# Optimization experiments

Measured on AMD Instinct MI355X. Metric: run time of the kernel, lower is better.

Reference implementation:

```python
import jax, jax.numpy as jnp
import numpy as np

B, T, C, H = 4, 2048, 1024, 16
HD = C // H


def setup_inputs() -> dict:
    key = jax.random.key(0)
    k1, k2, k3 = jax.random.split(key, 3)
    x = jax.random.normal(k1, (B, T, C), dtype=jnp.float32)
    w_attn = jax.random.normal(k2, (C, 3 * C), dtype=jnp.float32) * (1.0 / np.sqrt(C))
    b_attn = jnp.zeros((3 * C,), dtype=jnp.float32)
    w_proj = jax.random.normal(k3, (C, C), dtype=jnp.float32) * (1.0 / np.sqrt(C))
    b_proj = jnp.zeros((C,), dtype=jnp.float32)
    return {"x": x, "w_attn": w_attn, "b_attn": b_attn, "w_proj": w_proj, "b_proj": b_proj}


def reference(x, w_attn, b_attn, w_proj, b_proj):
    # QKV projection: [B,T,3C]
    qkv = x @ w_attn + b_attn
    q, k, v = jnp.split(qkv, 3, axis=-1)
    # [B,H,T,HD]
    q = q.reshape(B, T, H, HD).swapaxes(1, 2)
    k = k.reshape(B, T, H, HD).swapaxes(1, 2)
    v = v.reshape(B, T, H, HD).swapaxes(1, 2)
    scale = 1.0 / jnp.sqrt(jnp.float32(HD))
    attn = jnp.einsum('bhqd,bhkd->bhqk', q, k) * scale  # [B,H,T,T]
    causal = jnp.tril(jnp.ones((T, T), dtype=bool))
    attn = jnp.where(causal[None, None, :, :], attn, -jnp.inf)
    attn = jax.nn.softmax(attn, axis=-1)
    y = jnp.einsum('bhqk,bhkd->bhqd', attn, v)  # [B,H,T,HD]
    y = y.swapaxes(1, 2).reshape(B, T, C)
    return y @ w_proj + b_proj
```

## Files before the change

kernel.cpp:

```cpp
#include <hip/hip_runtime.h>
#include <hip/hip_bf16.h>

#define BB 4
#define TT 2048
#define CC 1024
#define HH 16
#define HD 64
#define NQ (3*CC)
#define QSCALE 0.18033688011112042f

typedef __attribute__((ext_vector_type(8))) short bf16x8;
typedef __attribute__((ext_vector_type(4))) short short4_t;
typedef __attribute__((ext_vector_type(4))) float f32x4;

#define MFMA(a,b,c) __builtin_amdgcn_mfma_f32_16x16x32_bf16(a,b,c,0,0,0)

#define ASYNC16(gsrc, ldst) \
  __builtin_amdgcn_global_load_lds((const __attribute__((address_space(1))) void*)(gsrc), \
                                   (__attribute__((address_space(3))) void*)(ldst), 16, 0, 0)

#define SWZA(row) (((((row) & 7) + (((row) >> 3) & 3)) & 7) << 3)

static __device__ __forceinline__ short f2bf(float f){
    union { float f; unsigned u; } v; v.f = f;
    unsigned r = v.u + 0x7FFFu + ((v.u >> 16) & 1u);
    return (short)(r >> 16);
}
static __device__ __forceinline__ unsigned cvtpk(float a, float b){
    unsigned r;
    asm("v_cvt_pk_bf16_f32 %0, %1, %2" : "=v"(r) : "v"(a), "v"(b));
    return r;
}

__global__ __launch_bounds__(256)
void convert_x(const float* __restrict__ x, short* __restrict__ xb)
{
    int i = (blockIdx.x * 256 + threadIdx.x) * 8;
    float4 a = *reinterpret_cast<const float4*>(&x[i]);
    float4 b = *reinterpret_cast<const float4*>(&x[i+4]);
    bf16x8 o = { f2bf(a.x), f2bf(a.y), f2bf(a.z), f2bf(a.w),
                 f2bf(b.x), f2bf(b.y), f2bf(b.z), f2bf(b.w) };
    *reinterpret_cast<bf16x8*>(&xb[i]) = o;
}

__global__ __launch_bounds__(256)
void transpose_w(const float* __restrict__ w, short* __restrict__ wT, int N)
{
    __shared__ short sm[64*72];
    const int kt0 = blockIdx.x * 64;
    const int nt0 = blockIdx.y * 64;
    const int t = threadIdx.x;
    const int r  = t >> 4;
    const int c4 = (t & 15) * 4;
#pragma unroll
    for (int it = 0; it < 4; it++){
        int k = r + it*16;
        float4 v = *reinterpret_cast<const float4*>(&w[(size_t)(kt0 + k)*N + nt0 + c4]);
        sm[(c4+0)*72 + k] = f2bf(v.x);
        sm[(c4+1)*72 + k] = f2bf(v.y);
        sm[(c4+2)*72 + k] = f2bf(v.z);
        sm[(c4+3)*72 + k] = f2bf(v.w);
    }
    __syncthreads();
    const int nl = t >> 2;
    const int kc = (t & 3) * 16;
    bf16x8 o0 = *reinterpret_cast<const bf16x8*>(&sm[nl*72 + kc]);
    bf16x8 o1 = *reinterpret_cast<const bf16x8*>(&sm[nl*72 + kc + 8]);
    short* dst = &wT[(size_t)(nt0 + nl)*CC + kt0 + kc];
    *reinterpret_cast<bf16x8*>(dst)     = o0;
    *reinterpret_cast<bf16x8*>(dst + 8) = o1;
}

__global__ __launch_bounds__(256)
void transpose_v(const short* __restrict__ vb, short* __restrict__ vtb)
{
    __shared__ short sm[64*72];
    const int bh = blockIdx.x;
    const int t0 = blockIdx.y * 64;
    const int t = threadIdx.x;
    const int r   = t >> 2;
    const int c16 = (t & 3) * 16;
    const short* src = vb + (size_t)bh*TT*HD + (size_t)t0*HD;
    bf16x8 a0 = *reinterpret_cast<const bf16x8*>(&src[r*HD + c16]);
    bf16x8 a1 = *reinterpret_cast<const bf16x8*>(&src[r*HD + c16 + 8]);
#pragma unroll
    for (int j=0;j<8;j++){
        sm[(c16+j)*72 + r]   = a0[j];
        sm[(c16+8+j)*72 + r] = a1[j];
    }
    __syncthreads();
    bf16x8 o0 = *reinterpret_cast<const bf16x8*>(&sm[r*72 + c16]);
    bf16x8 o1 = *reinterpret_cast<const bf16x8*>(&sm[r*72 + c16 + 8]);
    short* dst = vtb + (size_t)bh*HD*TT + (size_t)r*TT + t0 + c16;
    *reinterpret_cast<bf16x8*>(dst)     = o0;
    *reinterpret_cast<bf16x8*>(dst + 8) = o1;
}

__global__ __launch_bounds__(256, 2)
void qkv_gemm(const short* __restrict__ xb, const short* __restrict__ wT,
              const float* __restrict__ bias,
              short* __restrict__ qb, short* __restrict__ kb, short* __restrict__ vb)
{
    __shared__ short As[128*64];
    __shared__ short Bs[128*64];
    const int bid = blockIdx.x;
    const int swz = (bid & 7) * 192 + (bid >> 3);
    const int bm = swz / (NQ/128);
    const int bn = swz % (NQ/128);
    const int m0 = bm*128, n0 = bn*128;
    const int t  = threadIdx.x;
    const int wid = t >> 6, lane = t & 63;
    const int wr = wid >> 1, wc = wid & 1;
    const int l15 = lane & 15, lh = lane >> 4;

    f32x4 acc[4][4];
#pragma unroll
    for (int i=0;i<4;i++)
#pragma unroll
      for (int j=0;j<4;j++) acc[i][j] = (f32x4)0.f;

    for (int k0 = 0; k0 < CC; k0 += 64) {
        __syncthreads();
#pragma unroll
        for (int i=0;i<4;i++){
            int u   = (wid*4 + i)*64 + lane;
            int row = u >> 3, c = u & 7;
            int cs  = c ^ (row & 7);
            ASYNC16(&xb[(size_t)(m0+row)*CC + k0 + cs*8], &As[(wid*4+i)*512]);
            ASYNC16(&wT[(size_t)(n0+row)*CC + k0 + cs*8], &Bs[(wid*4+i)*512]);
        }
        __syncthreads();
#pragma unroll
        for (int ks=0;ks<2;ks++){
            bf16x8 a[4], b[4];
#pragma unroll
            for (int m=0;m<4;m++){
                int row = wr*64 + m*16 + l15;
                a[m] = *reinterpret_cast<const bf16x8*>(&As[row*64 + (((ks<<2)|lh) ^ (row&7))*8]);
            }
#pragma unroll
            for (int n=0;n<4;n++){
                int col = wc*64 + n*16 + l15;
                b[n] = *reinterpret_cast<const bf16x8*>(&Bs[col*64 + (((ks<<2)|lh) ^ (col&7))*8]);
            }
#pragma unroll
            for (int m=0;m<4;m++)
#pragma unroll
              for (int n=0;n<4;n++)
                acc[m][n] = MFMA(a[m], b[n], acc[m][n]);
        }
    }

#pragma unroll
    for (int n=0;n<4;n++){
        int col = n0 + wc*64 + n*16 + l15;
        int sect = col >> 10;
        int cc = col & 1023;
        int h = cc >> 6, d = cc & 63;
        float bv = bias[col];
        short* dst = (sect==0) ? qb : (sect==1) ? kb : vb;
        float mul = (sect==0) ? QSCALE : 1.f;
#pragma unroll
        for (int m=0;m<4;m++)
#pragma unroll
          for (int r=0;r<4;r++){
            int row = m0 + wr*64 + m*16 + lh*4 + r;
            int b_ = row >> 11, tt_ = row & (TT-1);
            float v = (acc[m][n][r] + bv) * mul;
            dst[((size_t)(b_*HH + h)*TT + tt_)*HD + d] = f2bf(v);
          }
    }
}

__global__ __launch_bounds__(256, 3)
void attn_kernel(const short* __restrict__ qb, const short* __restrict__ kb,
                 const short* __restrict__ vtb, short* __restrict__ yb)
{
    __shared__ short Ks[2][64*64];
    __shared__ short Vt[2][64*64];
    __shared__ short Ps[4][32*64];

    const int bh = blockIdx.x;
    const int qt = 15 - blockIdx.y;
    const int b_ = bh >> 4, h = bh & 15;
    const short* qp  = qb  + (size_t)bh*TT*HD;
    const short* kp  = kb  + (size_t)bh*TT*HD;
    const short* vtp = vtb + (size_t)bh*HD*TT;
    const int t = threadIdx.x, wid = t >> 6, lane = t & 63;
    const int l15 = lane & 15, lh = lane >> 4;

    int kvoffB[8];
#pragma unroll
    for (int ks=0;ks<2;ks++)
#pragma unroll
      for (int i=0;i<4;i++){
        int row = i*16 + l15;
        kvoffB[ks*4+i] = ((row*64 + ks*32 + lh*8) ^ SWZA(row)) * 2;
      }
    int pwB[8];
#pragma unroll
    for (int m=0;m<2;m++){
        int qloc = m*16 + l15;
#pragma unroll
        for (int f=0;f<4;f++)
            pwB[m*4+f] = ((qloc*64 + f*16 + lh*4) ^ SWZA(qloc)) * 2;
    }
    char* KsB = (char*)&Ks[0][0];
    char* VtB = (char*)&Vt[0][0];
    char* PsB = (char*)&Ps[wid][0];

    const int su0 = (wid*2+0)*64 + lane;
    const int su1 = (wid*2+1)*64 + lane;
    const int sr0 = su0 >> 3, sc0 = (su0 & 7) ^ (SWZA(su0 >> 3) >> 3);
    const int sr1 = su1 >> 3, sc1 = (su1 & 7) ^ (SWZA(su1 >> 3) >> 3);

    const short* kg0 = kp  + (size_t)sr0*HD + sc0*8;
    const short* kg1 = kp  + (size_t)sr1*HD + sc1*8;
    const short* vg0 = vtp + (size_t)sr0*TT + sc0*8;
    const short* vg1 = vtp + (size_t)sr1*TT + sc1*8;

    const bf16x8 ones = { 0x3F80,0x3F80,0x3F80,0x3F80,0x3F80,0x3F80,0x3F80,0x3F80 };

    auto stageN = [&](int buf){
        ASYNC16(kg0, &Ks[buf][(wid*2+0)*512]);
        ASYNC16(kg1, &Ks[buf][(wid*2+1)*512]);
        ASYNC16(vg0, &Vt[buf][(wid*2+0)*512]);
        ASYNC16(vg1, &Vt[buf][(wid*2+1)*512]);
        kg0 += 64*HD; kg1 += 64*HD; vg0 += 64; vg1 += 64;
    };

    const int wq0 = qt*128 + wid*32;

    bf16x8 qf[2][2];
#pragma unroll
    for (int m=0;m<2;m++)
#pragma unroll
      for (int ks=0;ks<2;ks++)
        qf[m][ks] = *reinterpret_cast<const bf16x8*>(
            &qp[(size_t)(wq0 + m*16 + l15)*HD + ks*32 + lh*8]);

    f32x4 po[2][4];
    f32x4 pden[2];
#pragma unroll
    for (int m=0;m<2;m++){
        pden[m] = (f32x4)0.f;
#pragma unroll
        for (int n=0;n<4;n++) po[m][n] = (f32x4)0.f;
    }

    const int ntk = 2*(qt + 1);

    stageN(0);
    __syncthreads();

    for (int kt = 0; kt < ntk; ){
#pragma unroll
        for (int cur = 0; cur < 2; cur++, kt++){
            const int kv0 = kt*64;
            if (kt+1 < ntk) stageN(cur ^ 1);

            if (kv0 <= wq0 + 31){
                f32x4 s[2][4];
#pragma unroll
                for (int m=0;m<2;m++)
#pragma unroll
                  for (int f=0;f<4;f++) s[m][f] = (f32x4)0.f;
                __builtin_amdgcn_s_setprio(1);
#pragma unroll
                for (int ks=0;ks<2;ks++){
#pragma unroll
                    for (int f=0;f<4;f++){
                        bf16x8 kf = *reinterpret_cast<const bf16x8*>(
                            KsB + cur*8192 + kvoffB[ks*4+f]);
                        s[0][f] = MFMA(kf, qf[0][ks], s[0][f]);
                        s[1][f] = MFMA(kf, qf[1][ks], s[1][f]);
                    }
                }
                __builtin_amdgcn_s_setprio(0);
#pragma unroll
                for (int m=0;m<2;m++){
                    if (kv0 + 63 > wq0 + m*16){
                        int qm = wq0 + m*16 + l15;
#pragma unroll
                        for (int f=0;f<4;f++)
#pragma unroll
                          for (int r=0;r<4;r++){
                            int kv = kv0 + f*16 + lh*4 + r;
                            if (kv > qm) s[m][f][r] = -1e30f;
                          }
                    }
                }
#pragma unroll
                for (int m=0;m<2;m++){
#pragma unroll
                    for (int f=0;f<4;f++){
                        uint2 pk;
                        pk.x = cvtpk(exp2f(s[m][f][0]), exp2f(s[m][f][1]));
                        pk.y = cvtpk(exp2f(s[m][f][2]), exp2f(s[m][f][3]));
                        *reinterpret_cast<uint2*>(PsB + pwB[m*4+f]) = pk;
                    }
                }
                __builtin_amdgcn_s_setprio(1);
#pragma unroll
                for (int k2=0;k2<2;k2++){
                    bf16x8 pa[2];
#pragma unroll
                    for (int m=0;m<2;m++)
                        pa[m] = *reinterpret_cast<const bf16x8*>(PsB + kvoffB[k2*4+m]);
                    pden[0] = MFMA(pa[0], ones, pden[0]);
                    pden[1] = MFMA(pa[1], ones, pden[1]);
#pragma unroll
                    for (int n=0;n<4;n++){
                        bf16x8 vf = *reinterpret_cast<const bf16x8*>(
                            VtB + cur*8192 + kvoffB[k2*4+n]);
                        po[0][n] = MFMA(pa[0], vf, po[0][n]);
                        po[1][n] = MFMA(pa[1], vf, po[1][n]);
                    }
                }
                __builtin_amdgcn_s_setprio(0);
            }

            __syncthreads();
        }
    }

#pragma unroll
    for (int m=0;m<2;m++){
        float rcp[4];
#pragma unroll
        for (int r=0;r<4;r++) rcp[r] = 1.f / pden[m][r];
#pragma unroll
        for (int n=0;n<4;n++)
#pragma unroll
          for (int r=0;r<4;r++){
            int q = wq0 + m*16 + lh*4 + r;
            int dd = n*16 + l15;
            yb[(size_t)(b_*TT + q)*CC + h*HD + dd] = f2bf(po[m][n][r] * rcp[r]);
          }
    }
}

__global__ __launch_bounds__(256, 2)
void proj_gemm(const short* __restrict__ y, const short* __restrict__ wpT,
               const float* __restrict__ bias, float* __restrict__ out)
{
    __shared__ short As[128*64];
    __shared__ short Bs[128*64];
    const int bid = blockIdx.x;
    const int swz = (bid & 7) * 64 + (bid >> 3);
    const int bm = swz >> 3, bn = swz & 7;
    const int m0 = bm*128, n0 = bn*128;
    const int t  = threadIdx.x;
    const int wid = t >> 6, lane = t & 63;
    const int wr = wid >> 1, wc = wid & 1;
    const int l15 = lane & 15, lh = lane >> 4;

    f32x4 acc[4][4];
#pragma unroll
    for (int i=0;i<4;i++)
#pragma unroll
      for (int j=0;j<4;j++) acc[i][j] = (f32x4)0.f;

    for (int k0 = 0; k0 < CC; k0 += 64) {
        __syncthreads();
#pragma unroll
        for (int i=0;i<4;i++){
            int u   = (wid*4 + i)*64 + lane;
            int row = u >> 3, c = u & 7;
            int cs  = c ^ (row & 7);
            ASYNC16(&y[(size_t)(m0+row)*CC + k0 + cs*8],   &As[(wid*4+i)*512]);
            ASYNC16(&wpT[(size_t)(n0+row)*CC + k0 + cs*8], &Bs[(wid*4+i)*512]);
        }
        __syncthreads();
#pragma unroll
        for (int ks=0;ks<2;ks++){
            bf16x8 a[4], b[4];
#pragma unroll
            for (int m=0;m<4;m++){
                int row = wr*64 + m*16 + l15;
                a[m] = *reinterpret_cast<const bf16x8*>(&As[row*64 + (((ks<<2)|lh) ^ (row&7))*8]);
            }
#pragma unroll
            for (int n=0;n<4;n++){
                int col = wc*64 + n*16 + l15;
                b[n] = *reinterpret_cast<const bf16x8*>(&Bs[col*64 + (((ks<<2)|lh) ^ (col&7))*8]);
            }
#pragma unroll
            for (int m=0;m<4;m++)
#pragma unroll
              for (int n=0;n<4;n++)
                acc[m][n] = MFMA(a[m], b[n], acc[m][n]);
        }
    }

#pragma unroll
    for (int n=0;n<4;n++){
        int col = n0 + wc*64 + n*16 + l15;
        float bv = bias[col];
#pragma unroll
        for (int m=0;m<4;m++)
#pragma unroll
          for (int r=0;r<4;r++){
            int row = m0 + wr*64 + m*16 + lh*4 + r;
            out[(size_t)row*CC + col] = acc[m][n][r] + bv;
          }
    }
}

extern "C" void kernel_launch(void* const* d_in, const int* in_sizes, int n_in,
                              void* d_out, int out_size, void* d_ws, size_t ws_size,
                              hipStream_t stream) {
    const float* x      = (const float*)d_in[0];
    const float* w_attn = (const float*)d_in[1];
    const float* b_attn = (const float*)d_in[2];
    const float* w_proj = (const float*)d_in[3];
    const float* b_proj = (const float*)d_in[4];
    float* out = (float*)d_out;

    const size_t S = (size_t)BB*TT*CC;
    short* qb  = (short*)d_ws;
    short* kb  = qb + S;
    short* vb  = kb + S;
    short* yx  = vb + S;
    short* wT  = yx + S;
    short* wpT = wT + (size_t)NQ*CC;
    short* vtb = wpT + (size_t)CC*CC;

    convert_x<<<dim3(S/(256*8)), 256, 0, stream>>>(x, yx);
    transpose_w<<<dim3(CC/64, NQ/64), 256, 0, stream>>>(w_attn, wT, NQ);
    transpose_w<<<dim3(CC/64, CC/64), 256, 0, stream>>>(w_proj, wpT, CC);
    qkv_gemm<<<dim3((BB*TT/128)*(NQ/128)), 256, 0, stream>>>(yx, wT, b_attn, qb, kb, vb);
    transpose_v<<<dim3(BB*HH, TT/64), 256, 0, stream>>>(vb, vtb);
    attn_kernel<<<dim3(BB*HH, TT/128), 256, 0, stream>>>(qb, kb, vtb, yx);
    proj_gemm<<<dim3((BB*TT/128)*(CC/128)), 256, 0, stream>>>(yx, wpT, b_proj, out);
}
```

Measured before the change: 180.0 us.

## Fuse V transpose into QKV GEMM epilogue and shrink attention P scratch

The QKV GEMM now writes V directly in transposed layout, staging the tile through shared memory, so the separate transpose_v kernel and its extra global round trip go away. The attention kernel's per-wave P buffer is halved to 16 rows: each m-slice is written and then immediately read back into registers. This lowers LDS use and lets launch bounds go up to 4 blocks per CU. The reuse of one P buffer across m-slices relies on write-then-read ordering within a wave, and the larger GEMM shared allocation may reduce that kernel's occupancy.

```diff
diff --git a/kernel.cpp b/kernel.cpp
--- a/kernel.cpp
+++ b/kernel.cpp
@@ -71,38 +71,14 @@
     *reinterpret_cast<bf16x8*>(dst + 8) = o1;
 }
 
-__global__ __launch_bounds__(256)
-void transpose_v(const short* __restrict__ vb, short* __restrict__ vtb)
-{
-    __shared__ short sm[64*72];
-    const int bh = blockIdx.x;
-    const int t0 = blockIdx.y * 64;
-    const int t = threadIdx.x;
-    const int r   = t >> 2;
-    const int c16 = (t & 3) * 16;
-    const short* src = vb + (size_t)bh*TT*HD + (size_t)t0*HD;
-    bf16x8 a0 = *reinterpret_cast<const bf16x8*>(&src[r*HD + c16]);
-    bf16x8 a1 = *reinterpret_cast<const bf16x8*>(&src[r*HD + c16 + 8]);
-#pragma unroll
-    for (int j=0;j<8;j++){
-        sm[(c16+j)*72 + r]   = a0[j];
-        sm[(c16+8+j)*72 + r] = a1[j];
-    }
-    __syncthreads();
-    bf16x8 o0 = *reinterpret_cast<const bf16x8*>(&sm[r*72 + c16]);
-    bf16x8 o1 = *reinterpret_cast<const bf16x8*>(&sm[r*72 + c16 + 8]);
-    short* dst = vtb + (size_t)bh*HD*TT + (size_t)r*TT + t0 + c16;
-    *reinterpret_cast<bf16x8*>(dst)     = o0;
-    *reinterpret_cast<bf16x8*>(dst + 8) = o1;
-}
-
 __global__ __launch_bounds__(256, 2)
 void qkv_gemm(const short* __restrict__ xb, const short* __restrict__ wT,
               const float* __restrict__ bias,
-              short* __restrict__ qb, short* __restrict__ kb, short* __restrict__ vb)
+              short* __restrict__ qb, short* __restrict__ kb, short* __restrict__ vtb)
 {
-    __shared__ short As[128*64];
-    __shared__ short Bs[128*64];
+    __shared__ short smem[128*136];
+    short* As = smem;
+    short* Bs = smem + 8192;
     const int bid = blockIdx.x;
     const int swz = (bid & 7) * 192 + (bid >> 3);
     const int bm = swz / (NQ/128);
@@ -151,34 +127,66 @@
         }
     }
 
-#pragma unroll
-    for (int n=0;n<4;n++){
-        int col = n0 + wc*64 + n*16 + l15;
-        int sect = col >> 10;
-        int cc = col & 1023;
-        int h = cc >> 6, d = cc & 63;
-        float bv = bias[col];
-        short* dst = (sect==0) ? qb : (sect==1) ? kb : vb;
-        float mul = (sect==0) ? QSCALE : 1.f;
-#pragma unroll
-        for (int m=0;m<4;m++)
-#pragma unroll
-          for (int r=0;r<4;r++){
-            int row = m0 + wr*64 + m*16 + lh*4 + r;
-            int b_ = row >> 11, tt_ = row & (TT-1);
-            float v = (acc[m][n][r] + bv) * mul;
-            dst[((size_t)(b_*HH + h)*TT + tt_)*HD + d] = f2bf(v);
-          }
-    }
-}
-
-__global__ __launch_bounds__(256, 3)
+    if (n0 < 2*CC) {
+#pragma unroll
+        for (int n=0;n<4;n++){
+            int col = n0 + wc*64 + n*16 + l15;
+            int sect = col >> 10;
+            int cc = col & 1023;
+            int h = cc >> 6, d = cc & 63;
+            float bv = bias[col];
+            short* dst = (sect==0) ? qb : kb;
+            float mul = (sect==0) ? QSCALE : 1.f;
+#pragma unroll
+            for (int m=0;m<4;m++)
+#pragma unroll
+              for (int r=0;r<4;r++){
+                int row = m0 + wr*64 + m*16 + lh*4 + r;
+                int b_ = row >> 11, tt_ = row & (TT-1);
+                float v = (acc[m][n][r] + bv) * mul;
+                dst[((size_t)(b_*HH + h)*TT + tt_)*HD + d] = f2bf(v);
+              }
+        }
+    } else {
+        __syncthreads();
+        short* Ts = smem;
+#pragma unroll
+        for (int n=0;n<4;n++){
+            int colL = wc*64 + n*16 + l15;
+            float bv = bias[n0 + colL];
+#pragma unroll
+            for (int m=0;m<4;m++){
+                int rowL = wr*64 + m*16 + lh*4;
+                short4_t pk = { f2bf(acc[m][n][0]+bv), f2bf(acc[m][n][1]+bv),
+                                f2bf(acc[m][n][2]+bv), f2bf(acc[m][n][3]+bv) };
+                *reinterpret_cast<short4_t*>(&Ts[colL*136 + rowL]) = pk;
+            }
+        }
+        __syncthreads();
+        const int b_ = m0 >> 11, t0 = m0 & (TT-1);
+        const int cc0 = n0 - 2*CC;
+#pragma unroll
+        for (int pass=0;pass<2;pass++){
+            int c = (t >> 2) + pass*64;
+            int vcol = cc0 + c;
+            short* dst = vtb + ((size_t)(b_*HH + (vcol>>6))*HD + (vcol&63))*TT + t0;
+#pragma unroll
+            for (int it=0;it<4;it++){
+                int r0 = (t & 3)*8 + it*32;
+                *reinterpret_cast<bf16x8*>(&dst[r0]) =
+                    *reinterpret_cast<const bf16x8*>(&Ts[c*136 + r0]);
+            }
+        }
+    }
+}
+
+__global__ __launch_bounds__(256, 4)
 void attn_kernel(const short* __restrict__ qb, const short* __restrict__ kb,
                  const short* __restrict__ vtb, short* __restrict__ yb)
 {
     __shared__ short Ks[2][64*64];
     __shared__ short Vt[2][64*64];
-    __shared__ short Ps[4][32*64];
+    __shared__ short Ps[4][16*64];
 
     const int bh = blockIdx.x;
     const int qt = 15 - blockIdx.y;
@@ -197,14 +205,10 @@
         int row = i*16 + l15;
         kvoffB[ks*4+i] = ((row*64 + ks*32 + lh*8) ^ SWZA(row)) * 2;
       }
-    int pwB[8];
-#pragma unroll
-    for (int m=0;m<2;m++){
-        int qloc = m*16 + l15;
-#pragma unroll
-        for (int f=0;f<4;f++)
-            pwB[m*4+f] = ((qloc*64 + f*16 + lh*4) ^ SWZA(qloc)) * 2;
-    }
+    int pwB[4];
+#pragma unroll
+    for (int f=0;f<4;f++)
+        pwB[f] = ((l15*64 + f*16 + lh*4) ^ SWZA(l15)) * 2;
     char* KsB = (char*)&Ks[0][0];
     char* VtB = (char*)&Vt[0][0];
     char* PsB = (char*)&Ps[wid][0];
@@ -290,6 +294,7 @@
                           }
                     }
                 }
+                bf16x8 pa[2][2];
 #pragma unroll
                 for (int m=0;m<2;m++){
 #pragma unroll
@@ -297,24 +302,22 @@
                         uint2 pk;
                         pk.x = cvtpk(exp2f(s[m][f][0]), exp2f(s[m][f][1]));
                         pk.y = cvtpk(exp2f(s[m][f][2]), exp2f(s[m][f][3]));
-                        *reinterpret_cast<uint2*>(PsB + pwB[m*4+f]) = pk;
+                        *reinterpret_cast<uint2*>(PsB + pwB[f]) = pk;
                     }
+                    pa[m][0] = *reinterpret_cast<const bf16x8*>(PsB + kvoffB[0]);
+                    pa[m][1] = *reinterpret_cast<const bf16x8*>(PsB + kvoffB[4]);
                 }
                 __builtin_amdgcn_s_setprio(1);
 #pragma unroll
                 for (int k2=0;k2<2;k2++){
-                    bf16x8 pa[2];
-#pragma unroll
-                    for (int m=0;m<2;m++)
-                        pa[m] = *reinterpret_cast<const bf16x8*>(PsB + kvoffB[k2*4+m]);
-                    pden[0] = MFMA(pa[0], ones, pden[0]);
-                    pden[1] = MFMA(pa[1], ones, pden[1]);
+                    pden[0] = MFMA(pa[0][k2], ones, pden[0]);
+                    pden[1] = MFMA(pa[1][k2], ones, pden[1]);
 #pragma unroll
                     for (int n=0;n<4;n++){
                         bf16x8 vf = *reinterpret_cast<const bf16x8*>(
                             VtB + cur*8192 + kvoffB[k2*4+n]);
-                        po[0][n] = MFMA(pa[0], vf, po[0][n]);
-                        po[1][n] = MFMA(pa[1], vf, po[1][n]);
+                        po[0][n] = MFMA(pa[0][k2], vf, po[0][n]);
+                        po[1][n] = MFMA(pa[1][k2], vf, po[1][n]);
                     }
                 }
                 __builtin_amdgcn_s_setprio(0);
@@ -420,17 +423,15 @@
     const size_t S = (size_t)BB*TT*CC;
     short* qb  = (short*)d_ws;
     short* kb  = qb + S;
-    short* vb  = kb + S;
-    short* yx  = vb + S;
+    short* vtb = kb + S;
+    short* yx  = vtb + S;
     short* wT  = yx + S;
     short* wpT = wT + (size_t)NQ*CC;
-    short* vtb = wpT + (size_t)CC*CC;
 
     convert_x<<<dim3(S/(256*8)), 256, 0, stream>>>(x, yx);
     transpose_w<<<dim3(CC/64, NQ/64), 256, 0, stream>>>(w_attn, wT, NQ);
     transpose_w<<<dim3(CC/64, CC/64), 256, 0, stream>>>(w_proj, wpT, CC);
-    qkv_gemm<<<dim3((BB*TT/128)*(NQ/128)), 256, 0, stream>>>(yx, wT, b_attn, qb, kb, vb);
-    transpose_v<<<dim3(BB*HH, TT/64), 256, 0, stream>>>(vb, vtb);
+    qkv_gemm<<<dim3((BB*TT/128)*(NQ/128)), 256, 0, stream>>>(yx, wT, b_attn, qb, kb, vtb);
     attn_kernel<<<dim3(BB*HH, TT/128), 256, 0, stream>>>(qb, kb, vtb, yx);
     proj_gemm<<<dim3((BB*TT/128)*(CC/128)), 256, 0, stream>>>(yx, wpT, b_proj, out);
 }
```

New measurement: 206.9 us. 1.15x slower.
